# Performance work log

Hardware: AMD Instinct MI355X
Metric: run time of the kernel (lower is better)

## Reference

```python
import jax, jax.numpy as jnp
import numpy as np

N, E, MUL, HID = 50000, 400000, 32, 64


def setup_inputs() -> dict:
    key = jax.random.key(0)
    ks = jax.random.split(key, 16)
    inp = {
        'node_scalars': jax.random.normal(ks[0], (N, MUL), jnp.float32),
        'node_vectors': jax.random.normal(ks[1], (N, MUL, 3), jnp.float32),
        'sh': jax.random.normal(ks[2], (E, 4), jnp.float32),
        'norm': jax.random.uniform(ks[3], (E, 1), jnp.float32),
        'mlp_w1': jax.random.normal(ks[4], (1, HID), jnp.float32),
        'mlp_b1': jnp.zeros((HID,), jnp.float32),
        'mlp_w2': jax.random.normal(ks[5], (HID, HID), jnp.float32) / np.sqrt(HID),
        'mlp_b2': jnp.zeros((HID,), jnp.float32),
        'mlp_w3': jax.random.normal(ks[6], (HID, 4 * MUL), jnp.float32) / np.sqrt(HID),
        'mlp_b3': jnp.zeros((4 * MUL,), jnp.float32),
        'lin1_w_s': jax.random.normal(ks[7], (2 * MUL, 6 * MUL), jnp.float32),
        'lin1_w_v': jax.random.normal(ks[8], (2 * MUL, 2 * MUL), jnp.float32),
        'lin2_w_s': jax.random.normal(ks[9], (5 * MUL, MUL), jnp.float32),
        'lin2_w_v': jax.random.normal(ks[10], (3 * MUL, MUL), jnp.float32),
        'senders': jax.random.randint(ks[11], (E,), 0, N, jnp.int32),
        'receivers': jax.random.randint(ks[12], (E,), 0, N, jnp.int32),
    }
    return inp


def reference(node_scalars, node_vectors, sh, norm,
              mlp_w1, mlp_b1, mlp_w2, mlp_b2, mlp_w3, mlp_b3,
              lin1_w_s, lin1_w_v, lin2_w_s, lin2_w_v,
              senders, receivers):
    n = node_scalars.shape[0]
    y0, y1 = sh[:, :1], sh[:, 1:]                      # 0e SH [E,1], 1o SH [E,3]
    # ---- gather sender features ----
    s_e = node_scalars[senders]                         # [E,MUL]
    v_e = node_vectors[senders]                         # [E,MUL,3]
    # ---- CG tensor product (sh 0e+1o) x (MULx0e + MULx1o) -> 2MULx0e + 2MULx1o ----
    tp_s = jnp.concatenate([y0 * s_e,
                            jnp.einsum('ek,emk->em', y1, v_e) / jnp.sqrt(3.0)], axis=-1)   # [E,2MUL]
    tp_v = jnp.concatenate([y0[:, :, None] * v_e,
                            y1[:, None, :] * s_e[:, :, None]], axis=1)                      # [E,2MUL,3]
    # ---- MLP on edge norms -> one gating scalar per output irrep (4MUL) ----
    h = jax.nn.silu(norm @ mlp_w1 + mlp_b1)
    h = jax.nn.silu(h @ mlp_w2 + mlp_b2)
    scal = h @ mlp_w3 + mlp_b3                          # [E,4MUL]
    m2 = tp_s.shape[-1]
    tp_s = tp_s * scal[:, :m2]
    tp_v = tp_v * scal[:, m2:, None]
    # ---- scatter-mean into receivers ----
    cnt = jax.ops.segment_sum(jnp.ones((receivers.shape[0],), tp_s.dtype), receivers, num_segments=n)
    denom = jnp.maximum(cnt, 1.0)[:, None]
    agg_s = jax.ops.segment_sum(tp_s, receivers, num_segments=n) / denom                    # [N,2MUL]
    agg_v = jax.ops.segment_sum(tp_v, receivers, num_segments=n) / denom[:, :, None]        # [N,2MUL,3]
    # ---- equivariant Linear -> irreps + gate scalars ----
    x_s = agg_s @ lin1_w_s / jnp.sqrt(jnp.float32(agg_s.shape[-1]))                         # [N,6MUL]
    x_v = jnp.einsum('nmi,mo->noi', agg_v, lin1_w_v) / jnp.sqrt(jnp.float32(agg_v.shape[1]))# [N,2MUL,3]
    n_vec = x_v.shape[1]
    act_s = jax.nn.silu(x_s[:, : x_s.shape[-1] - n_vec])                                    # [N,4MUL]
    gates = jax.nn.sigmoid(x_s[:, x_s.shape[-1] - n_vec:])                                  # [N,2MUL]
    g_v = x_v * gates[:, :, None]
    # ---- concat skip + final Linear to output irreps (MULx0e + MULx1o) ----
    c_s = jnp.concatenate([act_s, node_scalars], axis=-1)                                   # [N,5MUL]
    c_v = jnp.concatenate([g_v, node_vectors], axis=1)                                      # [N,3MUL,3]
    o_s = c_s @ lin2_w_s / jnp.sqrt(jnp.float32(c_s.shape[-1]))                             # [N,MUL]
    o_v = jnp.einsum('nmi,mo->noi', c_v, lin2_w_v) / jnp.sqrt(jnp.float32(c_v.shape[1]))    # [N,MUL,3]
    return jnp.concatenate([o_s, o_v.reshape(o_v.shape[0], -1)], axis=-1)                   # [N,4MUL]
```

## Files before the change

kernel.cpp:

```cpp
#include <hip/hip_runtime.h>

#define NN 50000
#define NE 400000
#define CNN 25000
#define NBINS 1024

#define RL1ST 0
#define RL1VT 12288
#define RL2S  16384
#define RL2V  21504
#define WTOT  24576

#define SLUT_N ((NBINS+1)*256)
#define N_INTS (3*NN+1+NE+512)

#define FULL_AGG_FL   ((size_t)NN*256)
#define FULL_TOT_FL   (FULL_AGG_FL + WTOT + SLUT_N + N_INTS)
#define WS_FULL_BYTES (FULL_TOT_FL*4ull)
#define CH_AGG_FL     ((size_t)CNN*256)
#define CH_TOT_FL     (CH_AGG_FL + WTOT + SLUT_N + N_INTS)
#define WS_CH_BYTES   (CH_TOT_FL*4ull)

#define SCAN_B 196

#define S160 0.07905694150420949f
#define S96  0.10206207261596576f

__device__ __forceinline__ float sigf(float x){
  return __builtin_amdgcn_rcpf(1.0f + __expf(-x));
}
__device__ __forceinline__ float siluf(float x){ return x * sigf(x); }

__global__ __launch_bounds__(256) void convert_weights(
    const float* __restrict__ l1s, const float* __restrict__ l1v,
    const float* __restrict__ l2s, const float* __restrict__ l2v,
    float* __restrict__ wgt)
{
  int i = blockIdx.x*256 + threadIdx.x;
  if (i < 12288){ int o=i>>6, m=i&63; wgt[RL1ST + i] = l1s[m*192+o]; return; }
  if (i < 16384){ int t=i-12288; int o=t>>6, m=t&63; wgt[RL1VT + t] = l1v[m*64+o]; return; }
  if (i < 21504){ int t=i-16384; wgt[RL2S + t] = l2s[t]; return; }
  if (i < 24576){ int t=i-21504; wgt[RL2V + t] = l2v[t]; return; }
}

__global__ __launch_bounds__(128) void build_lut(
    const float* __restrict__ w1, const float* __restrict__ b1,
    const float* __restrict__ w2, const float* __restrict__ b2,
    const float* __restrict__ w3, const float* __restrict__ b3,
    float* __restrict__ slut)
{
  __shared__ float h1[64], h2[64], scal[128];
  int bin = blockIdx.x;
  float x = (float)bin / (float)NBINS;
  int t = threadIdx.x;
  if (t < 64) h1[t] = siluf(fmaf(x, w1[t], b1[t]));
  __syncthreads();
  if (t < 64){
    float a = b2[t];
    for (int k=0;k<64;k++) a = fmaf(h1[k], w2[k*64+t], a);
    h2[t] = siluf(a);
  }
  __syncthreads();
  {
    float a = b3[t];
    for (int k=0;k<64;k++) a = fmaf(h2[k], w3[k*128+t], a);
    scal[t] = a;
  }
  __syncthreads();
  for (int c=t; c<256; c+=128){
    int m=c>>3, q=c&7;
    int idx = (q==0)? m : (q==1)? (32+m) : (q<5)? (64+m) : (96+m);
    slut[(size_t)bin*256 + c] = scal[idx];
  }
}

__global__ __launch_bounds__(256) void count_kernel(
    const int* __restrict__ rcv, int* __restrict__ cnt)
{
  int e = blockIdx.x*256 + threadIdx.x;
  if (e < NE) atomicAdd(&cnt[rcv[e]], 1);
}

__global__ __launch_bounds__(256) void scan_a(
    const int* __restrict__ cnt, int* __restrict__ offs, int* __restrict__ bsum)
{
  __shared__ int sd[256];
  int tid = threadIdx.x;
  int i = blockIdx.x*256 + tid;
  int c = (i < NN) ? cnt[i] : 0;
  sd[tid] = c;
  __syncthreads();
  for (int off=1; off<256; off<<=1){
    int t = (tid >= off) ? sd[tid-off] : 0;
    __syncthreads();
    sd[tid] += t;
    __syncthreads();
  }
  if (i < NN) offs[i] = sd[tid] - c;
  if (tid == 255) bsum[blockIdx.x] = sd[255];
}

__global__ __launch_bounds__(256) void scan_b(
    const int* __restrict__ bsum, int* __restrict__ bbase, int* __restrict__ offs)
{
  __shared__ int sd[256];
  int tid = threadIdx.x;
  int v = (tid < SCAN_B) ? bsum[tid] : 0;
  sd[tid] = v;
  __syncthreads();
  for (int off=1; off<256; off<<=1){
    int t = (tid >= off) ? sd[tid-off] : 0;
    __syncthreads();
    sd[tid] += t;
    __syncthreads();
  }
  if (tid < SCAN_B) bbase[tid] = sd[tid] - v;
  if (tid == 255) offs[NN] = sd[255];
}

__global__ __launch_bounds__(256) void scan_c(
    const int* __restrict__ bbase, int* __restrict__ offs, int* __restrict__ curs)
{
  int i = blockIdx.x*256 + threadIdx.x;
  if (i < NN){
    int o = offs[i] + bbase[blockIdx.x];
    offs[i] = o;
    curs[i] = o;
  }
}

__global__ __launch_bounds__(256) void scatter_kernel(
    const int* __restrict__ rcv, int* __restrict__ curs, int* __restrict__ eids)
{
  int e = blockIdx.x*256 + threadIdx.x;
  if (e >= NE) return;
  int pos = atomicAdd(&curs[rcv[e]], 1);
  eids[pos] = e;
}

__global__ __launch_bounds__(256) void edge_agg_kernel(
    const float* __restrict__ ns, const float* __restrict__ nv,
    const float* __restrict__ sh, const float* __restrict__ nrm,
    const int* __restrict__ snd,
    const int* __restrict__ offs, const int* __restrict__ eids,
    const float* __restrict__ slut,
    float* __restrict__ agg, int cn0, int cnn)
{
  int wave = threadIdx.x >> 6;
  int lane = threadIdx.x & 63;
  int nl = blockIdx.x*4 + wave;
  if (nl >= cnn) return;
  int n = cn0 + nl;
  int m = lane >> 1;
  int odd = lane & 1;
  int p0 = offs[n], p1 = offs[n+1];
  const float4* slut4 = (const float4*)slut;
  const float inv_sqrt3 = 0.57735026918962576f;
  float a0=0.f, a1=0.f, a2=0.f, a3=0.f;

  if (p0 < p1){
    const int plast = p1 - 1;
    int e0 = eids[p0];
    int s0 = snd[e0];
    float x0 = nrm[e0];
    float4 y0 = *(const float4*)(sh + 4*e0);
    float f0 = fminf(fmaxf(x0*(float)NBINS, 0.0f), (float)NBINS - 0.001f);
    int bin0 = (int)f0;
    float tt0 = f0 - (float)bin0;
    float4 La = slut4[(size_t)bin0*64 + lane];
    float4 Lb = slut4[(size_t)(bin0+1)*64 + lane];
    float se0 = ns[(size_t)s0*32 + m];
    const float* vp0 = nv + (size_t)s0*96 + 3*m;
    float v00 = vp0[0], v01 = vp0[1], v02 = vp0[2];
    int pm = (p0+1 <= plast) ? (p0+1) : plast;
    int e1 = eids[pm];
    int s1 = snd[e1];
    float x1 = nrm[e1];
    float4 y1 = *(const float4*)(sh + 4*e1);

    for (int p = p0; p <= plast; ++p){
      int pn = (p+2 <= plast) ? (p+2) : plast;
      int e2 = eids[pn];
      int s2 = snd[e2];
      float x2 = nrm[e2];
      float4 y2 = *(const float4*)(sh + 4*e2);
      float f1 = fminf(fmaxf(x1*(float)NBINS, 0.0f), (float)NBINS - 0.001f);
      int bin1 = (int)f1;
      float tt1 = f1 - (float)bin1;
      float4 La1 = slut4[(size_t)bin1*64 + lane];
      float4 Lb1 = slut4[(size_t)(bin1+1)*64 + lane];
      float se1 = ns[(size_t)s1*32 + m];
      const float* vp1 = nv + (size_t)s1*96 + 3*m;
      float v10 = vp1[0], v11 = vp1[1], v12 = vp1[2];

      float sc0 = fmaf(tt0, Lb.x-La.x, La.x);
      float sc1 = fmaf(tt0, Lb.y-La.y, La.y);
      float sc2 = fmaf(tt0, Lb.z-La.z, La.z);
      float sc3 = fmaf(tt0, Lb.w-La.w, La.w);
      float A0,A1,A2,A3;
      if (!odd){
        float dot = fmaf(y0.w, v02, fmaf(y0.z, v01, y0.y*v00));
        A0 = y0.x*se0; A1 = dot*inv_sqrt3; A2 = y0.x*v00; A3 = y0.x*v01;
      } else {
        A0 = y0.x*v02; A1 = y0.y*se0; A2 = y0.z*se0; A3 = y0.w*se0;
      }
      a0 = fmaf(A0, sc0, a0);
      a1 = fmaf(A1, sc1, a1);
      a2 = fmaf(A2, sc2, a2);
      a3 = fmaf(A3, sc3, a3);

      y0 = y1; tt0 = tt1;
      La = La1; Lb = Lb1;
      se0 = se1; v00 = v10; v01 = v11; v02 = v12;
      s1 = s2; x1 = x2; y1 = y2;
    }
  }
  int deg = p1 - p0;
  float inv = (deg > 0) ? __builtin_amdgcn_rcpf((float)deg) : 1.0f;
  float* ap = agg + (size_t)nl*256;
  int pos0 = odd ? (192+m) : m;
  int pos1 = odd ? ( 96+m) : (32+m);
  int pos2 = odd ? (160+m) : (64+m);
  int pos3 = odd ? (224+m) : (128+m);
  ap[pos0] = a0*inv;
  ap[pos1] = a1*inv;
  ap[pos2] = a2*inv;
  ap[pos3] = a3*inv;
}

__global__ __launch_bounds__(256) __attribute__((amdgpu_waves_per_eu(3,8)))
void node_s_kernel(
    const float* __restrict__ ns, const float* __restrict__ wgt,
    const float* __restrict__ agg, int cn0, int cnn,
    float* __restrict__ out)
{
  __shared__ float red[3*64*33];
  int lane = threadIdx.x & 63, role = threadIdx.x >> 6;
  int ro = __builtin_amdgcn_readfirstlane(role);
  int nl = blockIdx.x*64 + lane;
  bool valid = (nl < cnn);
  int nls = valid ? nl : (cnn-1);
  int n = cn0 + nl;

  float aggs[64];
  float oacc[32];
  #pragma unroll
  for (int j=0;j<32;j++) oacc[j]=0.0f;

  {
    const float4* ar = (const float4*)(agg + (size_t)nls*256);
    #pragma unroll
    for (int g=0; g<16; g++){
      float4 v = ar[g];
      aggs[4*g+0]=v.x; aggs[4*g+1]=v.y; aggs[4*g+2]=v.z; aggs[4*g+3]=v.w;
    }
  }
  const float* l1sT = wgt + RL1ST + ro*32*64;
  const float* l2s  = wgt + RL2S;
  for (int t=0;t<32;t++){
    const float4* col = (const float4*)(l1sT + t*64);
    float d0=0,d1=0,d2=0,d3=0;
    #pragma unroll
    for (int j=0;j<16;j++){
      float4 c = col[j];
      d0 = fmaf(aggs[4*j+0], c.x, d0);
      d1 = fmaf(aggs[4*j+1], c.y, d1);
      d2 = fmaf(aggs[4*j+2], c.z, d2);
      d3 = fmaf(aggs[4*j+3], c.w, d3);
    }
    float act = siluf(((d0+d1)+(d2+d3))*0.125f);
    const float4* row = (const float4*)(l2s + (size_t)(ro*32 + t)*32);
    #pragma unroll
    for (int j=0;j<8;j++){
      float4 w = row[j];
      oacc[4*j+0] = fmaf(act, w.x, oacc[4*j+0]);
      oacc[4*j+1] = fmaf(act, w.y, oacc[4*j+1]);
      oacc[4*j+2] = fmaf(act, w.z, oacc[4*j+2]);
      oacc[4*j+3] = fmaf(act, w.w, oacc[4*j+3]);
    }
  }
  {
    const float4* sp = (const float4*)(ns + (size_t)(cn0+nls)*32 + ro*8);
    #pragma unroll
    for (int q4=0;q4<2;q4++){
      float4 v = sp[q4];
      float vv[4] = {v.x, v.y, v.z, v.w};
      #pragma unroll
      for (int u=0;u<4;u++){
        int q = ro*8 + q4*4 + u;
        const float4* row = (const float4*)(l2s + (size_t)(128+q)*32);
        #pragma unroll
        for (int j=0;j<8;j++){
          float4 w = row[j];
          oacc[4*j+0] = fmaf(vv[u], w.x, oacc[4*j+0]);
          oacc[4*j+1] = fmaf(vv[u], w.y, oacc[4*j+1]);
          oacc[4*j+2] = fmaf(vv[u], w.z, oacc[4*j+2]);
          oacc[4*j+3] = fmaf(vv[u], w.w, oacc[4*j+3]);
        }
      }
    }
  }

  if (role != 0){
    float* rp = red + (role-1)*(64*33) + lane*33;
    #pragma unroll
    for (int j=0;j<32;j++) rp[j] = oacc[j];
  }
  __syncthreads();
  if (role == 0 && valid){
    #pragma unroll
    for (int j=0;j<32;j++)
      oacc[j] += red[0*(64*33)+lane*33+j] + red[1*(64*33)+lane*33+j]
               + red[2*(64*33)+lane*33+j];
    float4* op = (float4*)(out + (size_t)n*128);
    #pragma unroll
    for (int j=0;j<8;j++){
      float4 o4;
      o4.x = oacc[4*j+0]*S160; o4.y = oacc[4*j+1]*S160;
      o4.z = oacc[4*j+2]*S160; o4.w = oacc[4*j+3]*S160;
      op[j] = o4;
    }
  }
}

__global__ __launch_bounds__(192) __attribute__((amdgpu_waves_per_eu(3,8)))
void node_v_kernel(
    const float* __restrict__ nv, const float* __restrict__ wgt,
    const float* __restrict__ agg, int cn0, int cnn,
    float* __restrict__ out)
{
  __shared__ float sw[64*97];
  int lane = threadIdx.x & 63, role = threadIdx.x >> 6;
  int ro = __builtin_amdgcn_readfirstlane(role);
  int nl = blockIdx.x*64 + lane;
  bool valid = (nl < cnn);
  int nls = valid ? nl : (cnn-1);
  const float* arow = agg + (size_t)nls*256;

  {
    float aggs[64];
    const float4* ar = (const float4*)arow;
    #pragma unroll
    for (int g=0; g<16; g++){
      float4 v = ar[g];
      aggs[4*g+0]=v.x; aggs[4*g+1]=v.y; aggs[4*g+2]=v.z; aggs[4*g+3]=v.w;
    }
    const float* l1g = wgt + RL1ST + 128*64;
    for (int o=ro; o<64; o+=3){
      const float4* col = (const float4*)(l1g + o*64);
      float d0=0,d1=0,d2=0,d3=0;
      #pragma unroll
      for (int j=0;j<16;j++){
        float4 c = col[j];
        d0 = fmaf(aggs[4*j+0], c.x, d0);
        d1 = fmaf(aggs[4*j+1], c.y, d1);
        d2 = fmaf(aggs[4*j+2], c.z, d2);
        d3 = fmaf(aggs[4*j+3], c.w, d3);
      }
      sw[o*64+lane] = sigf(((d0+d1)+(d2+d3))*0.125f);
    }
  }
  __syncthreads();

  int k = role;
  float aggv[64], oacc[32];
  #pragma unroll
  for (int j=0;j<32;j++) oacc[j]=0.0f;
  {
    const float4* av = (const float4*)(arow + 64 + 64*k);
    #pragma unroll
    for (int g=0; g<16; g++){
      float4 v = av[g];
      aggv[4*g+0]=v.x; aggv[4*g+1]=v.y; aggv[4*g+2]=v.z; aggv[4*g+3]=v.w;
    }
  }
  const float* l1vT = wgt + RL1VT;
  const float* l2v  = wgt + RL2V;
  for (int o=0;o<64;o++){
    const float4* col = (const float4*)(l1vT + o*64);
    float d0=0,d1=0,d2=0,d3=0;
    #pragma unroll
    for (int j=0;j<16;j++){
      float4 c = col[j];
      d0 = fmaf(aggv[4*j+0], c.x, d0);
      d1 = fmaf(aggv[4*j+1], c.y, d1);
      d2 = fmaf(aggv[4*j+2], c.z, d2);
      d3 = fmaf(aggv[4*j+3], c.w, d3);
    }
    float gv = (((d0+d1)+(d2+d3))*0.125f) * sw[o*64+lane];
    const float4* row = (const float4*)(l2v + (size_t)o*32);
    #pragma unroll
    for (int j=0;j<8;j++){
      float4 w = row[j];
      oacc[4*j+0] = fmaf(gv, w.x, oacc[4*j+0]);
      oacc[4*j+1] = fmaf(gv, w.y, oacc[4*j+1]);
      oacc[4*j+2] = fmaf(gv, w.z, oacc[4*j+2]);
      oacc[4*j+3] = fmaf(gv, w.w, oacc[4*j+3]);
    }
  }
  {
    const float* vp = nv + (size_t)(cn0+nls)*96 + k;
    #pragma unroll 8
    for (int q=0;q<32;q++){
      float a = vp[3*q];
      const float4* row = (const float4*)(l2v + (size_t)(64+q)*32);
      #pragma unroll
      for (int j=0;j<8;j++){
        float4 w = row[j];
        oacc[4*j+0] = fmaf(a, w.x, oacc[4*j+0]);
        oacc[4*j+1] = fmaf(a, w.y, oacc[4*j+1]);
        oacc[4*j+2] = fmaf(a, w.z, oacc[4*j+2]);
        oacc[4*j+3] = fmaf(a, w.w, oacc[4*j+3]);
      }
    }
  }

  __syncthreads();
  if (valid){
    #pragma unroll
    for (int j=0;j<32;j++) sw[lane*97 + 3*j + k] = oacc[j]*S96;
  }
  __syncthreads();
  int nb = blockIdx.x*64;
  #pragma unroll
  for (int r=0;r<8;r++){
    int F = r*192 + threadIdx.x;
    int i = F/24, j = F%24;
    if (nb + i < cnn){
      float4 o4;
      o4.x = sw[i*97 + 4*j + 0];
      o4.y = sw[i*97 + 4*j + 1];
      o4.z = sw[i*97 + 4*j + 2];
      o4.w = sw[i*97 + 4*j + 3];
      *(float4*)(out + (size_t)(cn0+nb+i)*128 + 32 + 4*j) = o4;
    }
  }
}

extern "C" void kernel_launch(void* const* d_in, const int* in_sizes, int n_in,
                              void* d_out, int out_size, void* d_ws, size_t ws_size,
                              hipStream_t stream) {
  const float* node_scalars = (const float*)d_in[0];
  const float* node_vectors = (const float*)d_in[1];
  const float* sh           = (const float*)d_in[2];
  const float* norm         = (const float*)d_in[3];
  const float* w1  = (const float*)d_in[4];
  const float* b1  = (const float*)d_in[5];
  const float* w2  = (const float*)d_in[6];
  const float* b2  = (const float*)d_in[7];
  const float* w3  = (const float*)d_in[8];
  const float* b3  = (const float*)d_in[9];
  const float* l1s = (const float*)d_in[10];
  const float* l1v = (const float*)d_in[11];
  const float* l2s = (const float*)d_in[12];
  const float* l2v = (const float*)d_in[13];
  const int* snd = (const int*)d_in[14];
  const int* rcv = (const int*)d_in[15];
  float* ws = (float*)d_ws;
  float* out = (float*)d_out;

  if (ws_size < WS_CH_BYTES) return;

  bool full = (ws_size >= WS_FULL_BYTES);
  size_t aggfl = full ? FULL_AGG_FL : CH_AGG_FL;
  float* agg  = ws;
  float* wgt  = ws + aggfl;
  float* slut = wgt + WTOT;
  int*   ib   = (int*)(slut + SLUT_N);
  int* cnt  = ib;
  int* offs = ib + NN;
  int* curs = ib + 2*NN + 1;
  int* eids = ib + 3*NN + 1;
  int* bsum  = ib + 3*NN + 1 + NE;
  int* bbase = bsum + 256;

  hipMemsetAsync(cnt, 0, NN*sizeof(int), stream);

  convert_weights<<<(WTOT+255)/256, 256, 0, stream>>>(l1s, l1v, l2s, l2v, wgt);
  build_lut<<<NBINS+1, 128, 0, stream>>>(w1,b1,w2,b2,w3,b3, slut);

  count_kernel<<<(NE+255)/256, 256, 0, stream>>>(rcv, cnt);
  scan_a<<<SCAN_B, 256, 0, stream>>>(cnt, offs, bsum);
  scan_b<<<1, 256, 0, stream>>>(bsum, bbase, offs);
  scan_c<<<SCAN_B, 256, 0, stream>>>(bbase, offs, curs);
  scatter_kernel<<<(NE+255)/256, 256, 0, stream>>>(rcv, curs, eids);

  int nchunks = full ? 1 : 2;
  int csize   = full ? NN : CNN;
  for (int ch = 0; ch < nchunks; ch++){
    int cn0 = ch * csize;
    edge_agg_kernel<<<(csize+3)/4, 256, 0, stream>>>(
        node_scalars, node_vectors, sh, norm, snd, offs, eids, slut,
        agg, cn0, csize);
    node_s_kernel<<<(csize+63)/64, 256, 0, stream>>>(
        node_scalars, wgt, agg, cn0, csize, out);
    node_v_kernel<<<(csize+63)/64, 192, 0, stream>>>(
        node_vectors, wgt, agg, cn0, csize, out);
  }
}
```

Before: 349.6 us.

## Pack per-edge data in receiver-sorted order during scatter to remove indirection

The scatter kernel now writes sh, sender id and norm directly into receiver-sorted packed arrays (float4 plus int2), so the edge aggregation reads them contiguously instead of chasing eids into randomly ordered edge arrays. This removes one level of indirect, uncoalesced loads from the hot edge loop, at the cost of more random writes during scatter and extra workspace. Chunk sizing is also made adaptive to the available workspace.

```diff
diff --git a/kernel.cpp b/kernel.cpp
--- a/kernel.cpp
+++ b/kernel.cpp
@@ -2,7 +2,6 @@
 
 #define NN 50000
 #define NE 400000
-#define CNN 25000
 #define NBINS 1024
 
 #define RL1ST 0
@@ -12,14 +11,10 @@
 #define WTOT  24576
 
 #define SLUT_N ((NBINS+1)*256)
-#define N_INTS (3*NN+1+NE+512)
-
-#define FULL_AGG_FL   ((size_t)NN*256)
-#define FULL_TOT_FL   (FULL_AGG_FL + WTOT + SLUT_N + N_INTS)
-#define WS_FULL_BYTES (FULL_TOT_FL*4ull)
-#define CH_AGG_FL     ((size_t)CNN*256)
-#define CH_TOT_FL     (CH_AGG_FL + WTOT + SLUT_N + N_INTS)
-#define WS_CH_BYTES   (CH_TOT_FL*4ull)
+#define PK1_N  (4*NE)
+#define PK2_N  (2*NE)
+#define INTS_N 150528
+#define FIXED_FL ((size_t)WTOT + SLUT_N + PK1_N + PK2_N + INTS_N)
 
 #define SCAN_B 196
 
@@ -130,19 +125,22 @@
 }
 
 __global__ __launch_bounds__(256) void scatter_kernel(
-    const int* __restrict__ rcv, int* __restrict__ curs, int* __restrict__ eids)
+    const int* __restrict__ rcv, const int* __restrict__ snd,
+    const float* __restrict__ nrm, const float* __restrict__ sh,
+    int* __restrict__ curs,
+    float4* __restrict__ pk1, int2* __restrict__ pk2)
 {
   int e = blockIdx.x*256 + threadIdx.x;
   if (e >= NE) return;
   int pos = atomicAdd(&curs[rcv[e]], 1);
-  eids[pos] = e;
+  pk1[pos] = *(const float4*)(sh + 4*e);
+  pk2[pos] = make_int2(snd[e], __float_as_int(nrm[e]));
 }
 
 __global__ __launch_bounds__(256) void edge_agg_kernel(
     const float* __restrict__ ns, const float* __restrict__ nv,
-    const float* __restrict__ sh, const float* __restrict__ nrm,
-    const int* __restrict__ snd,
-    const int* __restrict__ offs, const int* __restrict__ eids,
+    const float4* __restrict__ pk1, const int2* __restrict__ pk2,
+    const int* __restrict__ offs,
     const float* __restrict__ slut,
     float* __restrict__ agg, int cn0, int cnn)
 {
@@ -160,10 +158,10 @@
 
   if (p0 < p1){
     const int plast = p1 - 1;
-    int e0 = eids[p0];
-    int s0 = snd[e0];
-    float x0 = nrm[e0];
-    float4 y0 = *(const float4*)(sh + 4*e0);
+    float4 y0 = pk1[p0];
+    int2  t0 = pk2[p0];
+    int   s0 = t0.x;
+    float x0 = __int_as_float(t0.y);
     float f0 = fminf(fmaxf(x0*(float)NBINS, 0.0f), (float)NBINS - 0.001f);
     int bin0 = (int)f0;
     float tt0 = f0 - (float)bin0;
@@ -173,17 +171,15 @@
     const float* vp0 = nv + (size_t)s0*96 + 3*m;
     float v00 = vp0[0], v01 = vp0[1], v02 = vp0[2];
     int pm = (p0+1 <= plast) ? (p0+1) : plast;
-    int e1 = eids[pm];
-    int s1 = snd[e1];
-    float x1 = nrm[e1];
-    float4 y1 = *(const float4*)(sh + 4*e1);
+    float4 y1 = pk1[pm];
+    int2  t1 = pk2[pm];
+    int   s1 = t1.x;
+    float x1 = __int_as_float(t1.y);
 
     for (int p = p0; p <= plast; ++p){
       int pn = (p+2 <= plast) ? (p+2) : plast;
-      int e2 = eids[pn];
-      int s2 = snd[e2];
-      float x2 = nrm[e2];
-      float4 y2 = *(const float4*)(sh + 4*e2);
+      float4 y2 = pk1[pn];
+      int2  t2 = pk2[pn];
       float f1 = fminf(fmaxf(x1*(float)NBINS, 0.0f), (float)NBINS - 0.001f);
       int bin1 = (int)f1;
       float tt1 = f1 - (float)bin1;
@@ -212,7 +208,7 @@
       y0 = y1; tt0 = tt1;
       La = La1; Lb = Lb1;
       se0 = se1; v00 = v10; v01 = v11; v02 = v12;
-      s1 = s2; x1 = x2; y1 = y2;
+      y1 = y2; s1 = t2.x; x1 = __int_as_float(t2.y);
     }
   }
   int deg = p1 - p0;
@@ -459,20 +455,24 @@
   float* ws = (float*)d_ws;
   float* out = (float*)d_out;
 
-  if (ws_size < WS_CH_BYTES) return;
-
-  bool full = (ws_size >= WS_FULL_BYTES);
-  size_t aggfl = full ? FULL_AGG_FL : CH_AGG_FL;
-  float* agg  = ws;
-  float* wgt  = ws + aggfl;
-  float* slut = wgt + WTOT;
-  int*   ib   = (int*)(slut + SLUT_N);
-  int* cnt  = ib;
-  int* offs = ib + NN;
-  int* curs = ib + 2*NN + 1;
-  int* eids = ib + 3*NN + 1;
-  int* bsum  = ib + 3*NN + 1 + NE;
+  size_t ws_fl = ws_size / 4;
+  if (ws_fl < FIXED_FL + 64*256) return;
+  size_t aggcap = ws_fl - FIXED_FL;
+  int csize = (int)((aggcap/256 < (size_t)NN) ? aggcap/256 : (size_t)NN);
+  csize &= ~63;
+  int nchunks = (NN + csize - 1) / csize;
+
+  float*  wgt  = ws;
+  float*  slut = wgt + WTOT;
+  float4* pk1  = (float4*)(slut + SLUT_N);
+  int2*   pk2  = (int2*)((float*)pk1 + PK1_N);
+  int*    ib   = (int*)((float*)pk2 + PK2_N);
+  int* cnt   = ib;
+  int* offs  = ib + NN;
+  int* curs  = ib + 2*NN + 1;
+  int* bsum  = ib + 3*NN + 1;
   int* bbase = bsum + 256;
+  float* agg = (float*)(ib + INTS_N);
 
   hipMemsetAsync(cnt, 0, NN*sizeof(int), stream);
 
@@ -483,18 +483,17 @@
   scan_a<<<SCAN_B, 256, 0, stream>>>(cnt, offs, bsum);
   scan_b<<<1, 256, 0, stream>>>(bsum, bbase, offs);
   scan_c<<<SCAN_B, 256, 0, stream>>>(bbase, offs, curs);
-  scatter_kernel<<<(NE+255)/256, 256, 0, stream>>>(rcv, curs, eids);
-
-  int nchunks = full ? 1 : 2;
-  int csize   = full ? NN : CNN;
+  scatter_kernel<<<(NE+255)/256, 256, 0, stream>>>(rcv, snd, norm, sh, curs, pk1, pk2);
+
   for (int ch = 0; ch < nchunks; ch++){
     int cn0 = ch * csize;
-    edge_agg_kernel<<<(csize+3)/4, 256, 0, stream>>>(
-        node_scalars, node_vectors, sh, norm, snd, offs, eids, slut,
-        agg, cn0, csize);
-    node_s_kernel<<<(csize+63)/64, 256, 0, stream>>>(
-        node_scalars, wgt, agg, cn0, csize, out);
-    node_v_kernel<<<(csize+63)/64, 192, 0, stream>>>(
-        node_vectors, wgt, agg, cn0, csize, out);
-  }
-}
+    int cnn = (NN - cn0 < csize) ? (NN - cn0) : csize;
+    edge_agg_kernel<<<(cnn+3)/4, 256, 0, stream>>>(
+        node_scalars, node_vectors, pk1, pk2, offs, slut,
+        agg, cn0, cnn);
+    node_s_kernel<<<(cnn+63)/64, 256, 0, stream>>>(
+        node_scalars, wgt, agg, cn0, cnn, out);
+    node_v_kernel<<<(cnn+63)/64, 192, 0, stream>>>(
+        node_vectors, wgt, agg, cn0, cnn, out);
+  }
+}
```

Result: slower. 446.3 us (+27.7%).

## Process nodes in descending degree order in edge aggregation, resize workspace chunks

Applied to the files above, without the earlier changes.

Adds a counting sort of the nodes by in-degree (histogram, scan, scatter) so the edge aggregation kernel handles high-degree nodes first. Each wave looks up its node through the sorted index, and nodes of similar degree sit together in a block. The aim is less load imbalance and tail effect from random degree variation. The workspace layout is reorganised so the chunk size comes from the available space, which may cut the number of chunks. It adds several small launches, scattered agg writes and an extra index indirection, and edits the edge-prefetch rotation (e1 = e2).

```diff
diff --git a/kernel.cpp b/kernel.cpp
--- a/kernel.cpp
+++ b/kernel.cpp
@@ -2,8 +2,8 @@
 
 #define NN 50000
 #define NE 400000
-#define CNN 25000
 #define NBINS 1024
+#define NSBIN 512
 
 #define RL1ST 0
 #define RL1VT 12288
@@ -12,14 +12,8 @@
 #define WTOT  24576
 
 #define SLUT_N ((NBINS+1)*256)
-#define N_INTS (3*NN+1+NE+512)
-
-#define FULL_AGG_FL   ((size_t)NN*256)
-#define FULL_TOT_FL   (FULL_AGG_FL + WTOT + SLUT_N + N_INTS)
-#define WS_FULL_BYTES (FULL_TOT_FL*4ull)
-#define CH_AGG_FL     ((size_t)CNN*256)
-#define CH_TOT_FL     (CH_AGG_FL + WTOT + SLUT_N + N_INTS)
-#define WS_CH_BYTES   (CH_TOT_FL*4ull)
+#define INTS_N (3*NN + 1 + NE + 1024)
+#define FIXED_FL ((size_t)WTOT + SLUT_N + INTS_N)
 
 #define SCAN_B 196
 
@@ -138,19 +132,62 @@
   eids[pos] = e;
 }
 
+__global__ __launch_bounds__(256) void dhist_kernel(
+    const int* __restrict__ offs, int* __restrict__ hist, int cn0, int cnn)
+{
+  int i = blockIdx.x*256 + threadIdx.x;
+  if (i < cnn){
+    int n = cn0 + i;
+    int d = offs[n+1] - offs[n];
+    int b = (d < NSBIN) ? (NSBIN-1-d) : 0;
+    atomicAdd(&hist[b], 1);
+  }
+}
+
+__global__ __launch_bounds__(512) void dhist_scan(int* __restrict__ hist)
+{
+  __shared__ int sd[512];
+  int t = threadIdx.x;
+  int v = hist[t];
+  sd[t] = v;
+  __syncthreads();
+  for (int off=1; off<512; off<<=1){
+    int x = (t >= off) ? sd[t-off] : 0;
+    __syncthreads();
+    sd[t] += x;
+    __syncthreads();
+  }
+  hist[t] = sd[t] - v;
+}
+
+__global__ __launch_bounds__(256) void dsort_kernel(
+    const int* __restrict__ offs, int* __restrict__ hist,
+    int* __restrict__ sorted, int cn0, int cnn)
+{
+  int i = blockIdx.x*256 + threadIdx.x;
+  if (i < cnn){
+    int n = cn0 + i;
+    int d = offs[n+1] - offs[n];
+    int b = (d < NSBIN) ? (NSBIN-1-d) : 0;
+    int pos = atomicAdd(&hist[b], 1);
+    sorted[cn0 + pos] = n;
+  }
+}
+
 __global__ __launch_bounds__(256) void edge_agg_kernel(
     const float* __restrict__ ns, const float* __restrict__ nv,
     const float* __restrict__ sh, const float* __restrict__ nrm,
     const int* __restrict__ snd,
     const int* __restrict__ offs, const int* __restrict__ eids,
+    const int* __restrict__ sorted,
     const float* __restrict__ slut,
     float* __restrict__ agg, int cn0, int cnn)
 {
   int wave = threadIdx.x >> 6;
   int lane = threadIdx.x & 63;
-  int nl = blockIdx.x*4 + wave;
-  if (nl >= cnn) return;
-  int n = cn0 + nl;
+  int nls = blockIdx.x*4 + wave;
+  if (nls >= cnn) return;
+  int n = sorted[cn0 + nls];
   int m = lane >> 1;
   int odd = lane & 1;
   int p0 = offs[n], p1 = offs[n+1];
@@ -212,12 +249,12 @@
       y0 = y1; tt0 = tt1;
       La = La1; Lb = Lb1;
       se0 = se1; v00 = v10; v01 = v11; v02 = v12;
-      s1 = s2; x1 = x2; y1 = y2;
+      e1 = e2; s1 = s2; x1 = x2; y1 = y2;
     }
   }
   int deg = p1 - p0;
   float inv = (deg > 0) ? __builtin_amdgcn_rcpf((float)deg) : 1.0f;
-  float* ap = agg + (size_t)nl*256;
+  float* ap = agg + (size_t)(n - cn0)*256;
   int pos0 = odd ? (192+m) : m;
   int pos1 = odd ? ( 96+m) : (32+m);
   int pos2 = odd ? (160+m) : (64+m);
@@ -459,20 +496,24 @@
   float* ws = (float*)d_ws;
   float* out = (float*)d_out;
 
-  if (ws_size < WS_CH_BYTES) return;
-
-  bool full = (ws_size >= WS_FULL_BYTES);
-  size_t aggfl = full ? FULL_AGG_FL : CH_AGG_FL;
-  float* agg  = ws;
-  float* wgt  = ws + aggfl;
+  size_t ws_fl = ws_size / 4;
+  if (ws_fl < FIXED_FL + 64*256) return;
+  size_t aggcap = (ws_fl - FIXED_FL) / 256;
+  int csize = (int)((aggcap < (size_t)NN) ? aggcap : (size_t)NN);
+  int nchunks = (NN + csize - 1) / csize;
+
+  float* wgt  = ws;
   float* slut = wgt + WTOT;
   int*   ib   = (int*)(slut + SLUT_N);
-  int* cnt  = ib;
-  int* offs = ib + NN;
-  int* curs = ib + 2*NN + 1;
-  int* eids = ib + 3*NN + 1;
-  int* bsum  = ib + 3*NN + 1 + NE;
-  int* bbase = bsum + 256;
+  int* offs   = ib;
+  int* curs   = ib + NN + 1;
+  int* eids   = ib + 2*NN + 1;
+  int* sorted = ib + 2*NN + 1 + NE;
+  int* cnt    = sorted;
+  int* hist   = ib + 3*NN + 1 + NE;
+  int* bsum   = hist + 512;
+  int* bbase  = bsum + 256;
+  float* agg  = (float*)(bbase + 256);
 
   hipMemsetAsync(cnt, 0, NN*sizeof(int), stream);
 
@@ -485,16 +526,20 @@
   scan_c<<<SCAN_B, 256, 0, stream>>>(bbase, offs, curs);
   scatter_kernel<<<(NE+255)/256, 256, 0, stream>>>(rcv, curs, eids);
 
-  int nchunks = full ? 1 : 2;
-  int csize   = full ? NN : CNN;
   for (int ch = 0; ch < nchunks; ch++){
     int cn0 = ch * csize;
-    edge_agg_kernel<<<(csize+3)/4, 256, 0, stream>>>(
-        node_scalars, node_vectors, sh, norm, snd, offs, eids, slut,
-        agg, cn0, csize);
-    node_s_kernel<<<(csize+63)/64, 256, 0, stream>>>(
-        node_scalars, wgt, agg, cn0, csize, out);
-    node_v_kernel<<<(csize+63)/64, 192, 0, stream>>>(
-        node_vectors, wgt, agg, cn0, csize, out);
-  }
-}
+    int cnn = (NN - cn0 < csize) ? (NN - cn0) : csize;
+    hipMemsetAsync(hist, 0, NSBIN*sizeof(int), stream);
+    dhist_kernel<<<(cnn+255)/256, 256, 0, stream>>>(offs, hist, cn0, cnn);
+    dhist_scan<<<1, 512, 0, stream>>>(hist);
+    dsort_kernel<<<(cnn+255)/256, 256, 0, stream>>>(offs, hist, sorted, cn0, cnn);
+
+    edge_agg_kernel<<<(cnn+3)/4, 256, 0, stream>>>(
+        node_scalars, node_vectors, sh, norm, snd, offs, eids, sorted, slut,
+        agg, cn0, cnn);
+    node_s_kernel<<<(cnn+63)/64, 256, 0, stream>>>(
+        node_scalars, wgt, agg, cn0, cnn, out);
+    node_v_kernel<<<(cnn+63)/64, 192, 0, stream>>>(
+        node_vectors, wgt, agg, cn0, cnn, out);
+  }
+}
```

Measured after the change: 701.2 us. 2.01x slower.
